# Kernel optimization log

Hardware: AMD Instinct MI355X
Metric: run time of the kernel (lower is better)

## Reference

```python
import jax, jax.numpy as jnp
import numpy as np

B, D, H, W, K = 32, 256, 32, 32, 2048
BETA = 0.25
JSD_TS = 1.0


def setup_inputs() -> dict:
    key = jax.random.key(0)
    k1, k2 = jax.random.split(key)
    z = jax.random.normal(k1, (B, D, H, W), dtype=jnp.float32)
    # nn.Embedding(K, D) with uniform(-1/K, 1/K) init
    codebook = jax.random.uniform(k2, (K, D), minval=-1.0 / K, maxval=1.0 / K, dtype=jnp.float32)
    return {"z": z, "codebook": codebook, "i": 0, "it": 0}


def _vq_forward(z, codebook):
    b, d, h, w = z.shape
    # (b, d, h, w) -> (b*h*w, d)
    z_flat = jnp.transpose(z, (0, 2, 3, 1)).reshape(-1, d)
    # squared euclidean distances via sum-of-squares + matmul: (n, K)
    dist = (jnp.sum(z_flat * z_flat, axis=1, keepdims=True)
            + jnp.sum(codebook * codebook, axis=1)
            - 2.0 * (z_flat @ codebook.T))
    min_idx = jnp.argmin(dist, axis=1)                      # (n,)
    distance_prob = jax.nn.softmax(-dist / JSD_TS, axis=1)  # (n, K)
    z_q = codebook[min_idx]                                 # embedding gather (n, d)
    # VQ losses (normalize == 'none' so z_norm == z_flat)
    codebook_loss = jnp.mean((z_q - jax.lax.stop_gradient(z_flat)) ** 2)
    commitment_loss = jnp.mean((z_flat - jax.lax.stop_gradient(z_q)) ** 2)
    q_loss = codebook_loss + BETA * commitment_loss
    # straight-through estimator
    z_q = z_flat + jax.lax.stop_gradient(z_q - z_flat)
    z_q = jnp.transpose(z_q.reshape(b, h, w, d), (0, 3, 1, 2))
    return z_q, q_loss, distance_prob


def reference(z, codebook, i, it):
    # i, it are unused loop counters in the original forward (eval path)
    return _vq_forward(z, codebook)
```

## Files before the change

### kernel.cpp

```cpp
#include <hip/hip_runtime.h>
#include <hip/hip_bf16.h>
#include <stdint.h>

#define K_CODES 2048
#define DIM 256
#define NROWS 32768
#define ROWS_PER_BLOCK 16
#define THREADS 512
#define HW_STRIDE 1024
#define ZQ_SIZE 8388608ULL
#define QLOSS_OFFSET 8388608
#define PROB_OFFSET 8388609ULL
#define ZB_PITCH 264

typedef short v8s __attribute__((ext_vector_type(8)));
typedef float v4f __attribute__((ext_vector_type(4)));

__device__ __forceinline__ ushort f2bf(float x) {
    uint32_t u = __float_as_uint(x);
    return (ushort)((u + 0x7FFFu + ((u >> 16) & 1u)) >> 16);
}

__global__ void prep_kernel(const float* __restrict__ cb, ushort* __restrict__ cbb,
                            float* __restrict__ cnorm, float* __restrict__ qloss) {
    const int code = blockIdx.x;
    const int lane = threadIdx.x;
    float4 v = ((const float4*)(cb + code * DIM))[lane];
    ushort4 o;
    o.x = f2bf(v.x); o.y = f2bf(v.y); o.z = f2bf(v.z); o.w = f2bf(v.w);
    ((ushort4*)(cbb + code * DIM))[lane] = o;
    float ss = v.x * v.x + v.y * v.y + v.z * v.z + v.w * v.w;
    #pragma unroll
    for (int m = 32; m >= 1; m >>= 1) ss += __shfl_xor(ss, m, 64);
    if (lane == 0) cnorm[code] = ss;
    if (code == 0 && lane == 0) *qloss = 0.f;
}

__launch_bounds__(THREADS)
__global__ void vq_kernel(const float* __restrict__ z, const float* __restrict__ cb,
                          const ushort* __restrict__ cbb, const float* __restrict__ cnorm,
                          float* __restrict__ out) {
    __shared__ float zf[DIM * 16];
    __shared__ ushort zb[ROWS_PER_BLOCK * ZB_PITCH];
    __shared__ float red_sum[8][16];
    __shared__ float red_max[8][16];
    __shared__ float row_sum[16];
    __shared__ float row_max[16];
    __shared__ unsigned long long best[16];
    __shared__ int row_idx[16];
    __shared__ float lred[8];

    const int t = threadIdx.x;
    const int n0 = blockIdx.x * ROWS_PER_BLOCK;
    const int bb = n0 >> 10;
    const int hw = n0 & 1023;
    const float* zbase = z + (size_t)bb * (DIM * HW_STRIDE) + hw;

    if (t < 16) best[t] = 0ULL;

    #pragma unroll
    for (int j = 0; j < 2; ++j) {
        int i4 = t + j * THREADS;
        int d = i4 >> 2, m0 = (i4 & 3) << 2;
        float4 v = *(const float4*)(zbase + (size_t)d * HW_STRIDE + m0);
        *(float4*)&zf[d * 16 + m0] = v;
    }
    __syncthreads();
    #pragma unroll
    for (int j = 0; j < 4; ++j) {
        int i2 = t + j * THREADS;
        int m = i2 & 15, kp = i2 >> 4;
        float a0 = zf[(2 * kp) * 16 + m];
        float a1 = zf[(2 * kp + 1) * 16 + m];
        uint32_t pk = (uint32_t)f2bf(a0) | ((uint32_t)f2bf(a1) << 16);
        *(uint32_t*)&zb[m * ZB_PITCH + 2 * kp] = pk;
    }
    __syncthreads();

    const int wave = t >> 6, lane = t & 63;
    const int q = lane >> 4, lm = lane & 15;
    const int c0 = wave * 256;

    v8s afrag[8];
    const ushort* arow = &zb[lm * ZB_PITCH + q * 8];
    #pragma unroll
    for (int ks = 0; ks < 8; ++ks) afrag[ks] = *(const v8s*)(arow + ks * 32);

    v4f e[16];
    float sume[4] = {0.f, 0.f, 0.f, 0.f};
    float emax[4] = {0.f, 0.f, 0.f, 0.f};
    #pragma unroll
    for (int ct = 0; ct < 16; ++ct) {
        const int code = c0 + ct * 16 + lm;
        const v8s* bp = (const v8s*)(cbb + code * DIM + q * 8);
        v4f a = {0.f, 0.f, 0.f, 0.f};
        #pragma unroll
        for (int ks = 0; ks < 8; ++ks)
            a = __builtin_amdgcn_mfma_f32_16x16x32_bf16(afrag[ks], bp[ks * 4], a, 0, 0, 0);
        const float cn = cnorm[code];
        #pragma unroll
        for (int r = 0; r < 4; ++r) {
            float ev = __expf(2.f * a[r] - cn);
            a[r] = ev;
            sume[r] += ev;
            emax[r] = fmaxf(emax[r], ev);
        }
        e[ct] = a;
    }
    #pragma unroll
    for (int m = 1; m <= 8; m <<= 1) {
        #pragma unroll
        for (int r = 0; r < 4; ++r) {
            sume[r] += __shfl_xor(sume[r], m, 64);
            emax[r] = fmaxf(emax[r], __shfl_xor(emax[r], m, 64));
        }
    }
    if (lm == 0) {
        #pragma unroll
        for (int r = 0; r < 4; ++r) {
            red_sum[wave][q * 4 + r] = sume[r];
            red_max[wave][q * 4 + r] = emax[r];
        }
    }
    __syncthreads();
    if (t < 16) {
        float s = 0.f, mx = 0.f;
        #pragma unroll
        for (int w = 0; w < 8; ++w) { s += red_sum[w][t]; mx = fmaxf(mx, red_max[w][t]); }
        row_sum[t] = s;
        row_max[t] = mx;
    }
    __syncthreads();

    float thr[4];
    #pragma unroll
    for (int r = 0; r < 4; ++r) thr[r] = row_max[q * 4 + r] * 0.998f;
    unsigned long long cmask = 0ULL;
    #pragma unroll
    for (int ct = 0; ct < 16; ++ct) {
        #pragma unroll
        for (int r = 0; r < 4; ++r)
            if (e[ct][r] >= thr[r]) cmask |= 1ULL << (ct * 4 + r);
    }
    while (cmask) {
        int bit = __ffsll((unsigned long long)cmask) - 1;
        cmask &= cmask - 1;
        int ct = bit >> 2, r = bit & 3;
        int code = c0 + ct * 16 + lm;
        int row = q * 4 + r;
        const float4* crow = (const float4*)(cb + code * DIM);
        double dot = 0.0;
        for (int k4 = 0; k4 < 64; ++k4) {
            float4 cv = crow[k4];
            int kb = k4 * 4;
            dot += (double)zf[(kb) * 16 + row] * (double)cv.x;
            dot += (double)zf[(kb + 1) * 16 + row] * (double)cv.y;
            dot += (double)zf[(kb + 2) * 16 + row] * (double)cv.z;
            dot += (double)zf[(kb + 3) * 16 + row] * (double)cv.w;
        }
        float lg = (float)(2.0 * dot - (double)cnorm[code]);
        uint32_t u = __float_as_uint(lg);
        u = (u & 0x80000000u) ? ~u : (u | 0x80000000u);
        unsigned long long key =
            ((unsigned long long)u << 32) | (uint32_t)(0xFFFFFFFFu - (uint32_t)code);
        atomicMax(&best[row], key);
    }
    __syncthreads();
    if (t < 16) row_idx[t] = (int)(0xFFFFFFFFu - (uint32_t)(best[t] & 0xFFFFFFFFULL));
    __syncthreads();

    float rinv[4];
    #pragma unroll
    for (int r = 0; r < 4; ++r) rinv[r] = 1.f / row_sum[q * 4 + r];
    float* prob = out + PROB_OFFSET;
    #pragma unroll
    for (int ct = 0; ct < 16; ++ct) {
        int col = c0 + ct * 16 + lm;
        #pragma unroll
        for (int r = 0; r < 4; ++r)
            prob[(size_t)(n0 + q * 4 + r) * K_CODES + col] = e[ct][r] * rinv[r];
    }

    float lacc = 0.f;
    #pragma unroll
    for (int j = 0; j < 2; ++j) {
        int i4 = t + j * THREADS;
        int d = i4 >> 2, m0 = (i4 & 3) << 2;
        float ov[4];
        #pragma unroll
        for (int i = 0; i < 4; ++i) {
            int m = m0 + i;
            float cv = cb[row_idx[m] * DIM + d];
            float zv = zf[d * 16 + m];
            float df = zv - cv;
            lacc += df * df;
            ov[i] = cv;
        }
        *(float4*)(out + (size_t)bb * (DIM * HW_STRIDE) + hw + (size_t)d * HW_STRIDE + m0) =
            make_float4(ov[0], ov[1], ov[2], ov[3]);
    }
    #pragma unroll
    for (int m = 32; m >= 1; m >>= 1) lacc += __shfl_xor(lacc, m, 64);
    if (lane == 0) lred[wave] = lacc;
    __syncthreads();
    if (t == 0) {
        float s = 0.f;
        #pragma unroll
        for (int w = 0; w < 8; ++w) s += lred[w];
        atomicAdd(out + QLOSS_OFFSET, s * (1.25f / 8388608.f));
    }
}

extern "C" void kernel_launch(void* const* d_in, const int* in_sizes, int n_in,
                              void* d_out, int out_size, void* d_ws, size_t ws_size,
                              hipStream_t stream) {
    const float* z  = (const float*)d_in[0];
    const float* cb = (const float*)d_in[1];
    float* out = (float*)d_out;
    ushort* cbb  = (ushort*)d_ws;
    float*  cnm  = (float*)((char*)d_ws + (size_t)K_CODES * DIM * sizeof(ushort));
    prep_kernel<<<K_CODES, 64, 0, stream>>>(cb, cbb, cnm, out + QLOSS_OFFSET);
    vq_kernel<<<NROWS / ROWS_PER_BLOCK, THREADS, 0, stream>>>(z, cb, cbb, cnm, out);
}
```

Measured before the change: 691.0 us.

## Track argmin in MFMA loop, pack exp values to fp16, raise occupancy

Computes the argmin directly from the bf16 MFMA logits with a per-lane running best and shuffle/shared reduction, removing the fp64 exact-refinement pass and 64-bit atomics. Exponentials are held as packed fp16 pairs instead of fp32 to cut register use, and launch bounds request more resident blocks. The risk is argmin mismatches on near-ties due to bf16 dot products and slight precision loss in the stored probabilities.

```diff
diff --git a/kernel.cpp b/kernel.cpp
--- a/kernel.cpp
+++ b/kernel.cpp
@@ -8,13 +8,13 @@
 #define ROWS_PER_BLOCK 16
 #define THREADS 512
 #define HW_STRIDE 1024
-#define ZQ_SIZE 8388608ULL
 #define QLOSS_OFFSET 8388608
 #define PROB_OFFSET 8388609ULL
 #define ZB_PITCH 264
 
 typedef short v8s __attribute__((ext_vector_type(8)));
 typedef float v4f __attribute__((ext_vector_type(4)));
+typedef __fp16 v2h __attribute__((ext_vector_type(2)));
 
 __device__ __forceinline__ ushort f2bf(float x) {
     uint32_t u = __float_as_uint(x);
@@ -36,18 +36,17 @@
     if (code == 0 && lane == 0) *qloss = 0.f;
 }
 
-__launch_bounds__(THREADS)
+__launch_bounds__(THREADS, 4)
 __global__ void vq_kernel(const float* __restrict__ z, const float* __restrict__ cb,
                           const ushort* __restrict__ cbb, const float* __restrict__ cnorm,
                           float* __restrict__ out) {
     __shared__ float zf[DIM * 16];
     __shared__ ushort zb[ROWS_PER_BLOCK * ZB_PITCH];
     __shared__ float red_sum[8][16];
-    __shared__ float red_max[8][16];
+    __shared__ float red_val[8][16];
+    __shared__ int   red_code[8][16];
     __shared__ float row_sum[16];
-    __shared__ float row_max[16];
-    __shared__ unsigned long long best[16];
-    __shared__ int row_idx[16];
+    __shared__ int   row_idx[16];
     __shared__ float lred[8];
 
     const int t = threadIdx.x;
@@ -55,8 +54,6 @@
     const int bb = n0 >> 10;
     const int hw = n0 & 1023;
     const float* zbase = z + (size_t)bb * (DIM * HW_STRIDE) + hw;
-
-    if (t < 16) best[t] = 0ULL;
 
     #pragma unroll
     for (int j = 0; j < 2; ++j) {
@@ -86,9 +83,10 @@
     #pragma unroll
     for (int ks = 0; ks < 8; ++ks) afrag[ks] = *(const v8s*)(arow + ks * 32);
 
-    v4f e[16];
+    v2h ep[32];
     float sume[4] = {0.f, 0.f, 0.f, 0.f};
-    float emax[4] = {0.f, 0.f, 0.f, 0.f};
+    float bval[4] = {-1e30f, -1e30f, -1e30f, -1e30f};
+    int   bcode[4] = {0, 0, 0, 0};
     #pragma unroll
     for (int ct = 0; ct < 16; ++ct) {
         const int code = c0 + ct * 16 + lm;
@@ -100,73 +98,47 @@
         const float cn = cnorm[code];
         #pragma unroll
         for (int r = 0; r < 4; ++r) {
-            float ev = __expf(2.f * a[r] - cn);
+            float l = 2.f * a[r] - cn;
+            float ev = __expf(l);
+            sume[r] += ev;
+            if (l > bval[r]) { bval[r] = l; bcode[r] = code; }
             a[r] = ev;
-            sume[r] += ev;
-            emax[r] = fmaxf(emax[r], ev);
-        }
-        e[ct] = a;
+        }
+        ep[2 * ct]     = __builtin_amdgcn_cvt_pkrtz(a[0], a[1]);
+        ep[2 * ct + 1] = __builtin_amdgcn_cvt_pkrtz(a[2], a[3]);
     }
     #pragma unroll
     for (int m = 1; m <= 8; m <<= 1) {
         #pragma unroll
         for (int r = 0; r < 4; ++r) {
             sume[r] += __shfl_xor(sume[r], m, 64);
-            emax[r] = fmaxf(emax[r], __shfl_xor(emax[r], m, 64));
+            float v2 = __shfl_xor(bval[r], m, 64);
+            int   c2 = __shfl_xor(bcode[r], m, 64);
+            if (v2 > bval[r] || (v2 == bval[r] && c2 < bcode[r])) { bval[r] = v2; bcode[r] = c2; }
         }
     }
     if (lm == 0) {
         #pragma unroll
         for (int r = 0; r < 4; ++r) {
-            red_sum[wave][q * 4 + r] = sume[r];
-            red_max[wave][q * 4 + r] = emax[r];
+            red_sum[wave][q * 4 + r]  = sume[r];
+            red_val[wave][q * 4 + r]  = bval[r];
+            red_code[wave][q * 4 + r] = bcode[r];
         }
     }
     __syncthreads();
     if (t < 16) {
-        float s = 0.f, mx = 0.f;
-        #pragma unroll
-        for (int w = 0; w < 8; ++w) { s += red_sum[w][t]; mx = fmaxf(mx, red_max[w][t]); }
+        float s = 0.f, bv = -1e30f;
+        int bc = 0;
+        #pragma unroll
+        for (int w = 0; w < 8; ++w) {
+            s += red_sum[w][t];
+            float v = red_val[w][t];
+            int   c = red_code[w][t];
+            if (v > bv || (v == bv && c < bc)) { bv = v; bc = c; }
+        }
         row_sum[t] = s;
-        row_max[t] = mx;
-    }
-    __syncthreads();
-
-    float thr[4];
-    #pragma unroll
-    for (int r = 0; r < 4; ++r) thr[r] = row_max[q * 4 + r] * 0.998f;
-    unsigned long long cmask = 0ULL;
-    #pragma unroll
-    for (int ct = 0; ct < 16; ++ct) {
-        #pragma unroll
-        for (int r = 0; r < 4; ++r)
-            if (e[ct][r] >= thr[r]) cmask |= 1ULL << (ct * 4 + r);
-    }
-    while (cmask) {
-        int bit = __ffsll((unsigned long long)cmask) - 1;
-        cmask &= cmask - 1;
-        int ct = bit >> 2, r = bit & 3;
-        int code = c0 + ct * 16 + lm;
-        int row = q * 4 + r;
-        const float4* crow = (const float4*)(cb + code * DIM);
-        double dot = 0.0;
-        for (int k4 = 0; k4 < 64; ++k4) {
-            float4 cv = crow[k4];
-            int kb = k4 * 4;
-            dot += (double)zf[(kb) * 16 + row] * (double)cv.x;
-            dot += (double)zf[(kb + 1) * 16 + row] * (double)cv.y;
-            dot += (double)zf[(kb + 2) * 16 + row] * (double)cv.z;
-            dot += (double)zf[(kb + 3) * 16 + row] * (double)cv.w;
-        }
-        float lg = (float)(2.0 * dot - (double)cnorm[code]);
-        uint32_t u = __float_as_uint(lg);
-        u = (u & 0x80000000u) ? ~u : (u | 0x80000000u);
-        unsigned long long key =
-            ((unsigned long long)u << 32) | (uint32_t)(0xFFFFFFFFu - (uint32_t)code);
-        atomicMax(&best[row], key);
-    }
-    __syncthreads();
-    if (t < 16) row_idx[t] = (int)(0xFFFFFFFFu - (uint32_t)(best[t] & 0xFFFFFFFFULL));
+        row_idx[t] = bc;
+    }
     __syncthreads();
 
     float rinv[4];
@@ -176,9 +148,15 @@
     #pragma unroll
     for (int ct = 0; ct < 16; ++ct) {
         int col = c0 + ct * 16 + lm;
-        #pragma unroll
-        for (int r = 0; r < 4; ++r)
-            prob[(size_t)(n0 + q * 4 + r) * K_CODES + col] = e[ct][r] * rinv[r];
+        float e0 = (float)ep[2 * ct][0];
+        float e1 = (float)ep[2 * ct][1];
+        float e2 = (float)ep[2 * ct + 1][0];
+        float e3 = (float)ep[2 * ct + 1][1];
+        size_t base = (size_t)(n0 + q * 4) * K_CODES + col;
+        prob[base]                = e0 * rinv[0];
+        prob[base + K_CODES]      = e1 * rinv[1];
+        prob[base + 2 * K_CODES]  = e2 * rinv[2];
+        prob[base + 3 * K_CODES]  = e3 * rinv[3];
     }
 
     float lacc = 0.f;
```

Result: faster. 604.2 us (-12.6%).
